# Kernel tuning notes

Hardware: AMD Instinct MI355X
Metric: run time of the kernel (lower is better)

The kernel has to match this reference:

```python
import jax, jax.numpy as jnp
import numpy as np

ROWS, COLS, H, W = 128, 128, 128, 128
B, C = 2, 16
DENSITY = 0.01  # classic Hough vote matrix is very sparse binary


def setup_inputs() -> dict:
    key = jax.random.key(0)
    k_img, k_vote = jax.random.split(key)
    image = jax.random.normal(k_img, (B, C, ROWS, COLS), dtype=jnp.float32)
    # sparse binary voting matrix, shape (rows, cols, h, w)
    vote_index = (jax.random.uniform(k_vote, (ROWS, COLS, H, W)) < DENSITY).astype(jnp.float32)
    return {"image": image, "vote_index": vote_index}


def reference(image, vote_index):
    rows, cols, h, w = vote_index.shape
    b, c = image.shape[0], image.shape[1]
    V = vote_index.reshape(rows * cols, h * w)          # (rows*cols, h*w)
    x = jax.nn.relu(image.reshape(b * c, rows * cols))  # (b*c, rows*cols)
    ht = (x @ V) / cols                                 # (b*c, h*w)
    return ht.reshape(b, c, h, w)
```

## Files before the change

kernel.cpp:

```cpp
#include <hip/hip_runtime.h>

constexpr int Mdim = 32;
constexpr int Kdim = 16384;
constexpr int Ndim = 16384;

constexpr int TPB = 256;

constexpr int KT     = 8;
constexpr int KC     = Kdim / KT;
constexpr int SLABS  = KC / 16;
constexpr int NT32   = Ndim / 32;
constexpr int NBLK   = NT32 * KT / 4;
constexpr int DEPTH  = 4;

typedef short bf16x8 __attribute__((ext_vector_type(8)));
typedef float f32x16 __attribute__((ext_vector_type(16)));

__device__ __forceinline__ short f32_to_bf16(float f) {
    union { float f; unsigned u; } c; c.f = f;
    unsigned u = c.u;
    u += 0x7fffu + ((u >> 16) & 1u);
    return (short)(u >> 16);
}

__global__ __launch_bounds__(TPB)
void build_xa(const float* __restrict__ image, short* __restrict__ xa) {
    const int g    = blockIdx.x * TPB + threadIdx.x;
    const int lane = g & 63;
    const int slab = g >> 6;
    const int m    = lane & 31;
    const int k    = slab * 16 + (lane >> 5) * 8;
    const float* src = image + (size_t)m * Kdim + k;

    bf16x8 o;
    #pragma unroll
    for (int j = 0; j < 8; ++j)
        o[j] = f32_to_bf16(fmaxf(src[j], 0.0f) * (1.0f / 128.0f));
    reinterpret_cast<bf16x8*>(xa)[g] = o;
}

__global__ __launch_bounds__(TPB, 4)
void ht_gemm(const short* __restrict__ xa,
             const float* __restrict__ vote,
             float* __restrict__ parts)
{
    const int tid  = threadIdx.x;
    const int lane = tid & 63;
    const int w    = tid >> 6;
    const int wv   = blockIdx.x * 4 + w;
    const int nt   = wv & (NT32 - 1);
    const int kch  = wv >> 9;
    const int k0   = kch * KC;

    const int col  = nt * 32 + (lane & 31);
    const int krow = (lane >> 5) * 8;

    const float* vbase = vote + (size_t)(k0 + krow) * Ndim + col;
    const short* abase = xa + ((size_t)(k0 / 16) * 64 + lane) * 8;

    f32x16 acc;
    #pragma unroll
    for (int i = 0; i < 16; ++i) acc[i] = 0.0f;

    float  bv[DEPTH][8];
    bf16x8 av[DEPTH];

    auto load = [&](int slot, int s) {
        const float* p = vbase + (size_t)s * 16 * Ndim;
        #pragma unroll
        for (int j = 0; j < 8; ++j)
            bv[slot][j] = __builtin_nontemporal_load(p + (size_t)j * Ndim);
        av[slot] = *reinterpret_cast<const bf16x8*>(abase + (size_t)s * 512);
    };
    auto comp = [&](int slot) {
        bf16x8 f;
        #pragma unroll
        for (int j = 0; j < 8; ++j) f[j] = f32_to_bf16(bv[slot][j]);
        acc = __builtin_amdgcn_mfma_f32_32x32x16_bf16(av[slot], f, acc, 0, 0, 0);
    };

    #pragma unroll
    for (int u = 0; u < DEPTH; ++u) load(u, u);
    for (int s = 0; s < SLABS; s += DEPTH) {
        #pragma unroll
        for (int u = 0; u < DEPTH; ++u) {
            comp(u);
            if (s + DEPTH + u < SLABS) load(u, s + DEPTH + u);
        }
    }

    float* pb = parts + (size_t)kch * ((size_t)Mdim * Ndim);
    const int rbase = 4 * (lane >> 5);
    #pragma unroll
    for (int r = 0; r < 16; ++r) {
        const int row = (r & 3) + 8 * (r >> 2) + rbase;
        pb[(size_t)row * Ndim + col] = acc[r];
    }
}

__global__ __launch_bounds__(TPB)
void ht_reduce(const float* __restrict__ parts, float* __restrict__ out, int nchunks) {
    const size_t i4 = (size_t)blockIdx.x * TPB + threadIdx.x;
    const float4* p = reinterpret_cast<const float4*>(parts) + i4;
    float4 s = make_float4(0.f, 0.f, 0.f, 0.f);
    constexpr size_t stride4 = (size_t)Mdim * Ndim / 4;
    for (int c = 0; c < nchunks; ++c) {
        const float4 v = p[(size_t)c * stride4];
        s.x += v.x; s.y += v.y; s.z += v.z; s.w += v.w;
    }
    reinterpret_cast<float4*>(out)[i4] = s;
}

__global__ __launch_bounds__(TPB)
void ht_gemm_atomic(const float* __restrict__ image, const float* __restrict__ vote,
                    float* __restrict__ out) {
    __shared__ float xsh[256 * Mdim];
    const int tid = threadIdx.x;
    const int ntile = blockIdx.x % 16;
    const int k0 = (blockIdx.x / 16) * 256;
    const int nn0 = ntile * 1024 + tid * 4;
    for (int idx = tid; idx < 256 * Mdim; idx += TPB) {
        const int kk = idx >> 5, m = idx & 31;
        xsh[idx] = fmaxf(image[(size_t)m * Kdim + (k0 + kk)], 0.0f) * (1.0f / 128.0f);
    }
    __syncthreads();
    float4 acc[Mdim];
    #pragma unroll
    for (int m = 0; m < Mdim; ++m) acc[m] = make_float4(0.f, 0.f, 0.f, 0.f);
    const float* vptr = vote + (size_t)k0 * Ndim + nn0;
    for (int kk = 0; kk < 256; ++kk) {
        const float4 v = *reinterpret_cast<const float4*>(vptr);
        vptr += Ndim;
        #pragma unroll
        for (int m = 0; m < Mdim; ++m) {
            const float s = xsh[kk * Mdim + m];
            acc[m].x = fmaf(s, v.x, acc[m].x); acc[m].y = fmaf(s, v.y, acc[m].y);
            acc[m].z = fmaf(s, v.z, acc[m].z); acc[m].w = fmaf(s, v.w, acc[m].w);
        }
    }
    #pragma unroll
    for (int m = 0; m < Mdim; ++m) {
        float* o = out + (size_t)m * Ndim + nn0;
        unsafeAtomicAdd(o + 0, acc[m].x); unsafeAtomicAdd(o + 1, acc[m].y);
        unsafeAtomicAdd(o + 2, acc[m].z); unsafeAtomicAdd(o + 3, acc[m].w);
    }
}

extern "C" void kernel_launch(void* const* d_in, const int* in_sizes, int n_in,
                              void* d_out, int out_size, void* d_ws, size_t ws_size,
                              hipStream_t stream) {
    const float* image = (const float*)d_in[0];
    const float* vote  = (const float*)d_in[1];
    float* out = (float*)d_out;

    const size_t xa_bytes    = (size_t)(Kdim / 16) * 64 * 8 * sizeof(short);
    const size_t chunk_bytes = (size_t)Mdim * Ndim * sizeof(float);

    if (xa_bytes + (size_t)KT * chunk_bytes > ws_size) {
        (void)hipMemsetAsync(out, 0, (size_t)out_size * sizeof(float), stream);
        ht_gemm_atomic<<<dim3(16 * 64), TPB, 0, stream>>>(image, vote, out);
        return;
    }

    short* xa    = (short*)d_ws;
    float* parts = (float*)((char*)d_ws + xa_bytes);

    build_xa<<<dim3((Kdim / 16) * 64 / TPB), TPB, 0, stream>>>(image, xa);
    ht_gemm<<<dim3(NBLK), TPB, 0, stream>>>(xa, vote, parts);
    ht_reduce<<<dim3((Mdim * Ndim) / (4 * TPB)), TPB, 0, stream>>>(parts, out, KT);
}
```

Baseline: 1.307 ms.

## Stage vote tiles into LDS with async global_load_lds double buffering

The GEMM kernel now uses 512-thread blocks that cooperatively stream 16x512 vote tiles into double-buffered shared memory via global_load_lds. Each wave then reads its columns from LDS and issues two MFMAs per stage. The K split is doubled to 16 chunks. The fp32-to-bf16 conversion is changed to truncation (a plain high-half shift), which is exact for the binary vote matrix. The intent is wider, coalesced 16-byte loads and latency hiding through async copies, in exchange for a barrier per stage and double the partial-sum traffic in the reduce step.

```diff
diff --git a/kernel.cpp b/kernel.cpp
--- a/kernel.cpp
+++ b/kernel.cpp
@@ -4,14 +4,14 @@
 constexpr int Kdim = 16384;
 constexpr int Ndim = 16384;
 
-constexpr int TPB = 256;
+constexpr int TPB  = 256;
+constexpr int GTPB = 512;
 
-constexpr int KT     = 8;
+constexpr int BN     = 512;
+constexpr int NB     = Ndim / BN;
+constexpr int KT     = 16;
 constexpr int KC     = Kdim / KT;
-constexpr int SLABS  = KC / 16;
-constexpr int NT32   = Ndim / 32;
-constexpr int NBLK   = NT32 * KT / 4;
-constexpr int DEPTH  = 4;
+constexpr int NSTAGE = KC / 16;
 
 typedef short bf16x8 __attribute__((ext_vector_type(8)));
 typedef float f32x16 __attribute__((ext_vector_type(16)));
@@ -39,62 +39,89 @@
     reinterpret_cast<bf16x8*>(xa)[g] = o;
 }
 
-__global__ __launch_bounds__(TPB, 4)
+__device__ __forceinline__ void glds16(const float* src, float* dst) {
+    __builtin_amdgcn_global_load_lds(
+        (const __attribute__((address_space(1))) void*)src,
+        (__attribute__((address_space(3))) void*)dst,
+        16, 0, 0);
+}
+
+__global__ __launch_bounds__(GTPB, 4)
 void ht_gemm(const short* __restrict__ xa,
              const float* __restrict__ vote,
              float* __restrict__ parts)
 {
+    __shared__ float vbuf[2][16 * BN];
+
     const int tid  = threadIdx.x;
     const int lane = tid & 63;
     const int w    = tid >> 6;
-    const int wv   = blockIdx.x * 4 + w;
-    const int nt   = wv & (NT32 - 1);
-    const int kch  = wv >> 9;
+    const int nb   = blockIdx.x & (NB - 1);
+    const int kch  = blockIdx.x >> 5;
     const int k0   = kch * KC;
+    const int n0   = nb * BN;
 
-    const int col  = nt * 32 + (lane & 31);
+    const int nlo  = lane & 31;
     const int krow = (lane >> 5) * 8;
+    const int r0   = 2 * w;
 
-    const float* vbase = vote + (size_t)(k0 + krow) * Ndim + col;
     const short* abase = xa + ((size_t)(k0 / 16) * 64 + lane) * 8;
 
-    f32x16 acc;
+    f32x16 acc0, acc1;
     #pragma unroll
-    for (int i = 0; i < 16; ++i) acc[i] = 0.0f;
+    for (int i = 0; i < 16; ++i) { acc0[i] = 0.0f; acc1[i] = 0.0f; }
 
-    float  bv[DEPTH][8];
-    bf16x8 av[DEPTH];
-
-    auto load = [&](int slot, int s) {
-        const float* p = vbase + (size_t)s * 16 * Ndim;
+    auto stage = [&](int buf, int s) {
+        const float* rp = vote + (size_t)(k0 + s * 16 + r0) * Ndim + n0;
         #pragma unroll
-        for (int j = 0; j < 8; ++j)
-            bv[slot][j] = __builtin_nontemporal_load(p + (size_t)j * Ndim);
-        av[slot] = *reinterpret_cast<const bf16x8*>(abase + (size_t)s * 512);
-    };
-    auto comp = [&](int slot) {
-        bf16x8 f;
-        #pragma unroll
-        for (int j = 0; j < 8; ++j) f[j] = f32_to_bf16(bv[slot][j]);
-        acc = __builtin_amdgcn_mfma_f32_32x32x16_bf16(av[slot], f, acc, 0, 0, 0);
+        for (int i = 0; i < 4; ++i) {
+            const float* src = rp + (size_t)(i >> 1) * Ndim + (i & 1) * 256 + lane * 4;
+            glds16(src, &vbuf[buf][(r0 + (i >> 1)) * BN + (i & 1) * 256]);
+        }
     };
 
-    #pragma unroll
-    for (int u = 0; u < DEPTH; ++u) load(u, u);
-    for (int s = 0; s < SLABS; s += DEPTH) {
+    stage(0, 0);
+    bf16x8 aC = *reinterpret_cast<const bf16x8*>(abase);
+
+    int cur = 0;
+    for (int s = 0; s < NSTAGE; ++s) {
+        bf16x8 aN = aC;
+        if (s + 1 < NSTAGE) {
+            stage(cur ^ 1, s + 1);
+            aN = *reinterpret_cast<const bf16x8*>(abase + (size_t)(s + 1) * 512);
+            asm volatile("s_waitcnt vmcnt(5)" ::: "memory");
+        } else {
+            asm volatile("s_waitcnt vmcnt(0)" ::: "memory");
+        }
+        __builtin_amdgcn_s_barrier();
+        asm volatile("" ::: "memory");
+
+        const float* vb = &vbuf[cur][krow * BN + w * 64 + nlo];
+        bf16x8 b0, b1;
         #pragma unroll
-        for (int u = 0; u < DEPTH; ++u) {
-            comp(u);
-            if (s + DEPTH + u < SLABS) load(u, s + DEPTH + u);
+        for (int j = 0; j < 8; ++j) {
+            union { float f; unsigned u; } c0, c1;
+            c0.f = vb[j * BN];
+            c1.f = vb[j * BN + 32];
+            b0[j] = (short)(c0.u >> 16);
+            b1[j] = (short)(c1.u >> 16);
         }
+        acc0 = __builtin_amdgcn_mfma_f32_32x32x16_bf16(aC, b0, acc0, 0, 0, 0);
+        acc1 = __builtin_amdgcn_mfma_f32_32x32x16_bf16(aC, b1, acc1, 0, 0, 0);
+
+        __builtin_amdgcn_s_barrier();
+        asm volatile("" ::: "memory");
+        aC = aN; cur ^= 1;
     }
 
     float* pb = parts + (size_t)kch * ((size_t)Mdim * Ndim);
+    const int c0    = n0 + w * 64 + nlo;
     const int rbase = 4 * (lane >> 5);
     #pragma unroll
     for (int r = 0; r < 16; ++r) {
         const int row = (r & 3) + 8 * (r >> 2) + rbase;
-        pb[(size_t)row * Ndim + col] = acc[r];
+        pb[(size_t)row * Ndim + c0]      = acc0[r];
+        pb[(size_t)row * Ndim + c0 + 32] = acc1[r];
     }
 }
 
@@ -166,6 +193,6 @@
     float* parts = (float*)((char*)d_ws + xa_bytes);
 
     build_xa<<<dim3((Kdim / 16) * 64 / TPB), TPB, 0, stream>>>(image, xa);
-    ht_gemm<<<dim3(NBLK), TPB, 0, stream>>>(xa, vote, parts);
+    ht_gemm<<<dim3(NB * KT), GTPB, 0, stream>>>(xa, vote, parts);
     ht_reduce<<<dim3((Mdim * Ndim) / (4 * TPB)), TPB, 0, stream>>>(parts, out, KT);
 }
```

Measured after the change: 1.323 ms. About the same (+1.2%).
